# Performance work log

Hardware: AMD Instinct MI355X
Metric: run time of the kernel (lower is better)

Reference implementation:

```python
import jax, jax.numpy as jnp
import numpy as np

N = 50000          # nodes
E = 1_600_000      # edges (avg degree 32)
G = 512            # graphs in batch
IN_DIM = 128
HID = 64


def setup_inputs() -> dict:
    key = jax.random.key(0)
    ks = jax.random.split(key, 9)
    x = jax.random.normal(ks[0], (N, IN_DIM), dtype=jnp.float32)
    edge_index = jax.random.randint(ks[1], (2, E), 0, N, dtype=jnp.int64)
    edge_attr = jax.random.uniform(ks[2], (E,), dtype=jnp.float32)
    batch = jnp.sort(jax.random.randint(ks[3], (N,), 0, G, dtype=jnp.int64))
    W1 = jax.random.normal(ks[4], (IN_DIM, HID), dtype=jnp.float32) / np.sqrt(IN_DIM)
    b1 = jnp.zeros((HID,), dtype=jnp.float32)
    W2 = jax.random.normal(ks[5], (HID, HID), dtype=jnp.float32) / np.sqrt(HID)
    b2 = jnp.zeros((HID,), dtype=jnp.float32)
    Wlin = jax.random.normal(ks[6], (HID, 1), dtype=jnp.float32) / np.sqrt(HID)
    blin = jnp.zeros((1,), dtype=jnp.float32)
    return {"x": x, "edge_index": edge_index, "edge_attr": edge_attr,
            "batch": batch, "W1": W1, "b1": b1, "W2": W2, "b2": b2,
            "Wlin": Wlin, "blin": blin}


def reference(x, edge_index, edge_attr, batch, W1, b1, W2, b2, Wlin, blin):
    n = x.shape[0]
    src, dst = edge_index[0], edge_index[1]
    # GCNConv: add self-loops with weight 1, symmetric normalization
    loop = jnp.arange(n)
    src_f = jnp.concatenate([src, loop])
    dst_f = jnp.concatenate([dst, loop])
    w = jnp.concatenate([edge_attr, jnp.ones((n,), x.dtype)])
    deg = jax.ops.segment_sum(w, dst_f, num_segments=n)
    dis = jnp.where(deg > 0, jax.lax.rsqrt(jnp.maximum(deg, 1e-12)), 0.0)
    norm = dis[src_f] * w * dis[dst_f]  # [E+N]

    def conv(h, W, b):
        hw = h @ W                          # [N, HID]
        msg = norm[:, None] * hw[src_f]     # [E+N, HID]
        return jax.ops.segment_sum(msg, dst_f, num_segments=n) + b

    h = jax.nn.relu(conv(x, W1, b1))
    h = conv(h, W2, b2)
    # global_mean_pool over graph ids
    counts = jax.ops.segment_sum(jnp.ones((n,), h.dtype), batch, num_segments=G)
    pooled = jax.ops.segment_sum(h, batch, num_segments=G) / jnp.maximum(counts, 1.0)[:, None]
    return pooled @ Wlin + blin  # [G, 1]
```

## Files before the change

kernel.cpp:

```cpp
#include <hip/hip_runtime.h>

#define NN 50000
#define NE 1600000
#define NG 512
#define IN_DIM 128
#define HID 64

#define NB 128
#define NBK ((NN + NB - 1) / NB)
#define EBLK 250
#define EPB (NE / EBLK)
#define EPB4 (EPB / 4)

typedef unsigned short ushort_t;
typedef unsigned int uint_t;

static __device__ __forceinline__ ushort_t f2bf(float f) {
    uint_t u = __float_as_uint(f);
    u += 0x7FFFu + ((u >> 16) & 1u);
    return (ushort_t)(u >> 16);
}
static __device__ __forceinline__ float bflo(uint_t u) { return __uint_as_float(u << 16); }
static __device__ __forceinline__ float bfhi(uint_t u) { return __uint_as_float(u & 0xFFFF0000u); }

__global__ void cnt_kernel(const int* __restrict__ ei, int* __restrict__ pcnt) {
    __shared__ int h[NBK];
    for (int i = threadIdx.x; i < NBK; i += blockDim.x) h[i] = 0;
    __syncthreads();
    const int4* d4 = (const int4*)(ei + NE + blockIdx.x * EPB);
    for (int i = threadIdx.x; i < EPB4; i += blockDim.x) {
        int4 d = d4[i];
        atomicAdd(&h[d.x >> 7], 1);
        atomicAdd(&h[d.y >> 7], 1);
        atomicAdd(&h[d.z >> 7], 1);
        atomicAdd(&h[d.w >> 7], 1);
    }
    __syncthreads();
    for (int i = threadIdx.x; i < NBK; i += blockDim.x)
        pcnt[(size_t)i * EBLK + blockIdx.x] = h[i];
}

__global__ void bscan_kernel(int* __restrict__ pcnt, int* __restrict__ tot) {
    __shared__ int s[256];
    int k = blockIdx.x, t = threadIdx.x;
    int v = (t < EBLK) ? pcnt[(size_t)k * EBLK + t] : 0;
    s[t] = v;
    __syncthreads();
    for (int off = 1; off < 256; off <<= 1) {
        int add = (t >= off) ? s[t - off] : 0;
        __syncthreads();
        s[t] += add;
        __syncthreads();
    }
    if (t < EBLK) pcnt[(size_t)k * EBLK + t] = s[t] - v;
    if (t == 255) tot[k] = s[255];
}

__global__ void tscan_kernel(const int* __restrict__ tot, int* __restrict__ bbase) {
    __shared__ int s[512];
    int t = threadIdx.x;
    int v = (t < NBK) ? tot[t] : 0;
    s[t] = v;
    __syncthreads();
    for (int off = 1; off < 512; off <<= 1) {
        int add = (t >= off) ? s[t - off] : 0;
        __syncthreads();
        s[t] += add;
        __syncthreads();
    }
    if (t < NBK) bbase[t] = s[t] - v;
    if (t == NBK - 1) bbase[NBK] = s[t];
}

__global__ void scatter_kernel(const int* __restrict__ ei, const float* __restrict__ ea,
                               const int* __restrict__ pcnt, const int* __restrict__ bbase,
                               int2* __restrict__ recs) {
    __shared__ int curs[NBK];
    int b = blockIdx.x;
    for (int i = threadIdx.x; i < NBK; i += blockDim.x)
        curs[i] = bbase[i] + pcnt[(size_t)i * EBLK + b];
    __syncthreads();
    int base = b * EPB;
    const int4*   s4 = (const int4*)(ei + base);
    const int4*   d4 = (const int4*)(ei + NE + base);
    const float4* e4 = (const float4*)(ea + base);
    for (int i = threadIdx.x; i < EPB4; i += blockDim.x) {
        int4 ss = s4[i];
        int4 dd = d4[i];
        float4 ee = e4[i];
        int pos, k;
        k = dd.x >> 7; pos = atomicAdd(&curs[k], 1);
        recs[pos] = make_int2(((dd.x & 127) << 17) | ss.x, __float_as_int(ee.x));
        k = dd.y >> 7; pos = atomicAdd(&curs[k], 1);
        recs[pos] = make_int2(((dd.y & 127) << 17) | ss.y, __float_as_int(ee.y));
        k = dd.z >> 7; pos = atomicAdd(&curs[k], 1);
        recs[pos] = make_int2(((dd.z & 127) << 17) | ss.z, __float_as_int(ee.z));
        k = dd.w >> 7; pos = atomicAdd(&curs[k], 1);
        recs[pos] = make_int2(((dd.w & 127) << 17) | ss.w, __float_as_int(ee.w));
    }
}

__global__ void binfo2_kernel(const int2* __restrict__ recs, const int* __restrict__ bbase,
                              int* __restrict__ indeg, float* __restrict__ dis,
                              int* __restrict__ offs, int2* __restrict__ csr) {
    __shared__ float deg[NB];
    __shared__ int cnt[NB];
    __shared__ int sc[NB];
    __shared__ int curs[NB];
    __shared__ float wdst[NB];
    int k = blockIdx.x;
    int lo = k * NB;
    int nLoc = min(NB, NN - lo);
    int tid = threadIdx.x;
    for (int i = tid; i < nLoc; i += blockDim.x) { deg[i] = 0.f; cnt[i] = 0; }
    __syncthreads();
    int start = bbase[k], end = bbase[k + 1];
    for (int e = start + tid; e < end; e += blockDim.x) {
        int2 r = recs[e];
        int dl = r.x >> 17;
        atomicAdd(&deg[dl], __int_as_float(r.y));
        atomicAdd(&cnt[dl], 1);
    }
    __syncthreads();
    for (int i = tid; i < nLoc; i += blockDim.x) {
        float d = rsqrtf(deg[i] + 1.0f);
        wdst[i] = d;
        dis[lo + i] = d;
        indeg[lo + i] = cnt[i];
    }
    if (tid < NB) sc[tid] = (tid < nLoc) ? cnt[tid] : 0;
    __syncthreads();
    for (int off = 1; off < NB; off <<= 1) {
        int add = (tid < NB && tid >= off) ? sc[tid - off] : 0;
        __syncthreads();
        if (tid < NB) sc[tid] += add;
        __syncthreads();
    }
    if (tid < nLoc) {
        int ex = start + sc[tid] - cnt[tid];
        offs[lo + tid] = ex;
        curs[tid] = ex;
    }
    __syncthreads();
    for (int e = start + tid; e < end; e += blockDim.x) {
        int2 r = recs[e];
        int src = r.x & 0x1FFFF;
        int dl = r.x >> 17;
        float pw = __int_as_float(r.y) * wdst[dl];
        int pos = atomicAdd(&curs[dl], 1);
        csr[pos] = make_int2(src, __float_as_int(pw));
    }
}

template <int K>
__global__ __launch_bounds__(256) void gemm_kernel(const float* __restrict__ X,
                                                   const float* __restrict__ W,
                                                   const float* __restrict__ dis,
                                                   ushort_t* __restrict__ Yb) {
    __shared__ float w_lds[K * HID];
    __shared__ float x_lds[K][65];
    int tid = threadIdx.x;
    int rowbase = blockIdx.x * 64;
    for (int i = tid; i < K * HID; i += 256) w_lds[i] = W[i];
    for (int i = tid; i < 16 * K; i += 256) {
        int row = i / (K / 4);
        int k4 = i % (K / 4);
        int r = rowbase + row;
        float4 v = (r < NN) ? ((const float4*)(X + (size_t)r * K))[k4]
                            : make_float4(0.f, 0.f, 0.f, 0.f);
        x_lds[k4 * 4 + 0][row] = v.x;
        x_lds[k4 * 4 + 1][row] = v.y;
        x_lds[k4 * 4 + 2][row] = v.z;
        x_lds[k4 * 4 + 3][row] = v.w;
    }
    __syncthreads();
    int c0 = (tid & 15) * 4;
    int r0 = (tid >> 4) * 4;
    float acc[4][4] = {};
#pragma unroll 4
    for (int k = 0; k < K; ++k) {
        float x0 = x_lds[k][r0 + 0];
        float x1 = x_lds[k][r0 + 1];
        float x2 = x_lds[k][r0 + 2];
        float x3 = x_lds[k][r0 + 3];
        float4 wv = *(const float4*)&w_lds[k * HID + c0];
        acc[0][0] += x0 * wv.x; acc[0][1] += x0 * wv.y; acc[0][2] += x0 * wv.z; acc[0][3] += x0 * wv.w;
        acc[1][0] += x1 * wv.x; acc[1][1] += x1 * wv.y; acc[1][2] += x1 * wv.z; acc[1][3] += x1 * wv.w;
        acc[2][0] += x2 * wv.x; acc[2][1] += x2 * wv.y; acc[2][2] += x2 * wv.z; acc[2][3] += x2 * wv.w;
        acc[3][0] += x3 * wv.x; acc[3][1] += x3 * wv.y; acc[3][2] += x3 * wv.z; acc[3][3] += x3 * wv.w;
    }
#pragma unroll
    for (int i = 0; i < 4; ++i) {
        int r = rowbase + r0 + i;
        if (r < NN) {
            float dr = dis[r];
            ushort4 o;
            o.x = f2bf(dr * acc[i][0]); o.y = f2bf(dr * acc[i][1]);
            o.z = f2bf(dr * acc[i][2]); o.w = f2bf(dr * acc[i][3]);
            *(ushort4*)&Yb[(size_t)r * HID + c0] = o;
        }
    }
}

__global__ void gather1_kernel(const int2* __restrict__ csr,
                               const int* __restrict__ offs,
                               const int* __restrict__ indeg,
                               const float* __restrict__ dis,
                               const ushort_t* __restrict__ A1,
                               const float* __restrict__ b1,
                               float* __restrict__ OUT) {
    int node = blockIdx.x * 4 + (threadIdx.x >> 6);
    int lane = threadIdx.x & 63;
    if (node >= NN) return;
    int o  = lane >> 3;
    int cl = lane & 7;
    int start = offs[node];
    int n = indeg[node];
    float a0 = 0.f, a1 = 0.f, a2 = 0.f, a3 = 0.f;
    float a4 = 0.f, a5 = 0.f, a6 = 0.f, a7 = 0.f;
    for (int c = 0; c < n; c += 64) {
        int idx = c + lane;
        int2 rec = (idx < n) ? csr[start + idx] : make_int2(0, 0);
        int tmax = min(n - c, 64);
#pragma unroll 2
        for (int t = 0; t * 8 < tmax; ++t) {
            int sl = t * 8 + o;
            int key = __shfl(rec.x, sl, 64);
            float w = __int_as_float(__shfl(rec.y, sl, 64));
            uint4 v = *(const uint4*)(A1 + ((size_t)key << 6) + (cl << 3));
            a0 += w * bflo(v.x); a1 += w * bfhi(v.x);
            a2 += w * bflo(v.y); a3 += w * bfhi(v.y);
            a4 += w * bflo(v.z); a5 += w * bfhi(v.z);
            a6 += w * bflo(v.w); a7 += w * bfhi(v.w);
        }
    }
    a0 += __shfl_xor(a0, 8, 64); a0 += __shfl_xor(a0, 16, 64); a0 += __shfl_xor(a0, 32, 64);
    a1 += __shfl_xor(a1, 8, 64); a1 += __shfl_xor(a1, 16, 64); a1 += __shfl_xor(a1, 32, 64);
    a2 += __shfl_xor(a2, 8, 64); a2 += __shfl_xor(a2, 16, 64); a2 += __shfl_xor(a2, 32, 64);
    a3 += __shfl_xor(a3, 8, 64); a3 += __shfl_xor(a3, 16, 64); a3 += __shfl_xor(a3, 32, 64);
    a4 += __shfl_xor(a4, 8, 64); a4 += __shfl_xor(a4, 16, 64); a4 += __shfl_xor(a4, 32, 64);
    a5 += __shfl_xor(a5, 8, 64); a5 += __shfl_xor(a5, 16, 64); a5 += __shfl_xor(a5, 32, 64);
    a6 += __shfl_xor(a6, 8, 64); a6 += __shfl_xor(a6, 16, 64); a6 += __shfl_xor(a6, 32, 64);
    a7 += __shfl_xor(a7, 8, 64); a7 += __shfl_xor(a7, 16, 64); a7 += __shfl_xor(a7, 32, 64);
    if (o == 0) {
        float d = dis[node];
        uint4 sv = *(const uint4*)(A1 + ((size_t)node << 6) + (cl << 3));
        const float4* bv = (const float4*)(b1 + (cl << 3));
        float4 bA = bv[0], bB = bv[1];
        float o0 = fmaxf(a0 + d * bflo(sv.x) + bA.x, 0.f);
        float o1 = fmaxf(a1 + d * bfhi(sv.x) + bA.y, 0.f);
        float o2 = fmaxf(a2 + d * bflo(sv.y) + bA.z, 0.f);
        float o3 = fmaxf(a3 + d * bfhi(sv.y) + bA.w, 0.f);
        float o4 = fmaxf(a4 + d * bflo(sv.z) + bB.x, 0.f);
        float o5 = fmaxf(a5 + d * bfhi(sv.z) + bB.y, 0.f);
        float o6 = fmaxf(a6 + d * bflo(sv.w) + bB.z, 0.f);
        float o7 = fmaxf(a7 + d * bfhi(sv.w) + bB.w, 0.f);
        float* op = &OUT[((size_t)node << 6) + (cl << 3)];
        *(float4*)op       = make_float4(o0, o1, o2, o3);
        *(float4*)(op + 4) = make_float4(o4, o5, o6, o7);
    }
}

__global__ void gather2_kernel(const int2* __restrict__ csr,
                               const int* __restrict__ offs,
                               const int* __restrict__ indeg,
                               const float* __restrict__ dis,
                               const ushort_t* __restrict__ A2,
                               const float* __restrict__ b2,
                               const float* __restrict__ Wlin,
                               float* __restrict__ nodeval) {
    int node = blockIdx.x * 4 + (threadIdx.x >> 6);
    int lane = threadIdx.x & 63;
    if (node >= NN) return;
    int o  = lane >> 3;
    int cl = lane & 7;
    int start = offs[node];
    int n = indeg[node];
    float a0 = 0.f, a1 = 0.f, a2 = 0.f, a3 = 0.f;
    float a4 = 0.f, a5 = 0.f, a6 = 0.f, a7 = 0.f;
    for (int c = 0; c < n; c += 64) {
        int idx = c + lane;
        int2 rec = (idx < n) ? csr[start + idx] : make_int2(0, 0);
        int tmax = min(n - c, 64);
#pragma unroll 2
        for (int t = 0; t * 8 < tmax; ++t) {
            int sl = t * 8 + o;
            int key = __shfl(rec.x, sl, 64);
            float w = __int_as_float(__shfl(rec.y, sl, 64));
            uint4 v = *(const uint4*)(A2 + ((size_t)key << 6) + (cl << 3));
            a0 += w * bflo(v.x); a1 += w * bfhi(v.x);
            a2 += w * bflo(v.y); a3 += w * bfhi(v.y);
            a4 += w * bflo(v.z); a5 += w * bfhi(v.z);
            a6 += w * bflo(v.w); a7 += w * bfhi(v.w);
        }
    }
    a0 += __shfl_xor(a0, 8, 64); a0 += __shfl_xor(a0, 16, 64); a0 += __shfl_xor(a0, 32, 64);
    a1 += __shfl_xor(a1, 8, 64); a1 += __shfl_xor(a1, 16, 64); a1 += __shfl_xor(a1, 32, 64);
    a2 += __shfl_xor(a2, 8, 64); a2 += __shfl_xor(a2, 16, 64); a2 += __shfl_xor(a2, 32, 64);
    a3 += __shfl_xor(a3, 8, 64); a3 += __shfl_xor(a3, 16, 64); a3 += __shfl_xor(a3, 32, 64);
    a4 += __shfl_xor(a4, 8, 64); a4 += __shfl_xor(a4, 16, 64); a4 += __shfl_xor(a4, 32, 64);
    a5 += __shfl_xor(a5, 8, 64); a5 += __shfl_xor(a5, 16, 64); a5 += __shfl_xor(a5, 32, 64);
    a6 += __shfl_xor(a6, 8, 64); a6 += __shfl_xor(a6, 16, 64); a6 += __shfl_xor(a6, 32, 64);
    a7 += __shfl_xor(a7, 8, 64); a7 += __shfl_xor(a7, 16, 64); a7 += __shfl_xor(a7, 32, 64);
    float d = dis[node];
    uint4 sv = *(const uint4*)(A2 + ((size_t)node << 6) + (cl << 3));
    const float4* bv = (const float4*)(b2 + (cl << 3));
    float4 bA = bv[0], bB = bv[1];
    const float4* wv = (const float4*)(Wlin + (cl << 3));
    float4 wA = wv[0], wB = wv[1];
    float dot = (a0 + d * bflo(sv.x) + bA.x) * wA.x
              + (a1 + d * bfhi(sv.x) + bA.y) * wA.y
              + (a2 + d * bflo(sv.y) + bA.z) * wA.z
              + (a3 + d * bfhi(sv.y) + bA.w) * wA.w
              + (a4 + d * bflo(sv.z) + bB.x) * wB.x
              + (a5 + d * bfhi(sv.z) + bB.y) * wB.y
              + (a6 + d * bflo(sv.w) + bB.z) * wB.z
              + (a7 + d * bfhi(sv.w) + bB.w) * wB.w;
    dot += __shfl_xor(dot, 1, 64);
    dot += __shfl_xor(dot, 2, 64);
    dot += __shfl_xor(dot, 4, 64);
    if (lane == 0) nodeval[node] = dot;
}

__global__ void pool_final_kernel(const float* __restrict__ nodeval,
                                  const int* __restrict__ batch,
                                  const float* __restrict__ blin,
                                  float* __restrict__ out) {
    __shared__ int bnd[2];
    __shared__ float red[4];
    int g = blockIdx.x;
    if (threadIdx.x < 2) {
        int target = g + threadIdx.x;
        int lo = 0, hi = NN;
        while (lo < hi) {
            int mid = (lo + hi) >> 1;
            if (batch[mid] < target) lo = mid + 1; else hi = mid;
        }
        bnd[threadIdx.x] = lo;
    }
    __syncthreads();
    int s = bnd[0], e = bnd[1];
    float a = 0.f;
    for (int i = s + threadIdx.x; i < e; i += 256) a += nodeval[i];
    for (int off = 32; off > 0; off >>= 1) a += __shfl_down(a, off, 64);
    int lane = threadIdx.x & 63;
    int wv = threadIdx.x >> 6;
    if (lane == 0) red[wv] = a;
    __syncthreads();
    if (threadIdx.x == 0) {
        float t = red[0] + red[1] + red[2] + red[3];
        out[g] = t / fmaxf((float)(e - s), 1.0f) + blin[0];
    }
}

extern "C" void kernel_launch(void* const* d_in, const int* in_sizes, int n_in,
                              void* d_out, int out_size, void* d_ws, size_t ws_size,
                              hipStream_t stream) {
    const float* x     = (const float*)d_in[0];
    const int*   ei    = (const int*)d_in[1];
    const float* ea    = (const float*)d_in[2];
    const int*   batch = (const int*)d_in[3];
    const float* W1    = (const float*)d_in[4];
    const float* b1    = (const float*)d_in[5];
    const float* W2    = (const float*)d_in[6];
    const float* b2    = (const float*)d_in[7];
    const float* Wlin  = (const float*)d_in[8];
    const float* blin  = (const float*)d_in[9];
    float*       out   = (float*)d_out;

    char* ws = (char*)d_ws;
    auto alloc = [&](size_t bytes) {
        void* p = (void*)ws;
        ws += (bytes + 255) / 256 * 256;
        return p;
    };
    float*    dis     = (float*)alloc((size_t)NN * 4);
    int*      indeg   = (int*)alloc((size_t)NN * 4);
    int*      offs    = (int*)alloc((size_t)NN * 4);
    int*      pcnt    = (int*)alloc((size_t)NBK * EBLK * 4);
    int*      tot     = (int*)alloc((size_t)NBK * 4);
    int*      bbase   = (int*)alloc((size_t)(NBK + 1) * 4);
    int2*     recs    = (int2*)alloc((size_t)NE * 8);
    int2*     csr     = (int2*)alloc((size_t)NE * 8);
    float*    B       = (float*)alloc((size_t)NN * HID * 4);
    float*    nodeval = (float*)alloc((size_t)NN * 4);
    ushort_t* A1      = (ushort_t*)recs;
    ushort_t* A2      = (ushort_t*)recs + (size_t)NN * HID;

    cnt_kernel<<<EBLK, 256, 0, stream>>>(ei, pcnt);
    bscan_kernel<<<NBK, 256, 0, stream>>>(pcnt, tot);
    tscan_kernel<<<1, 512, 0, stream>>>(tot, bbase);
    scatter_kernel<<<EBLK, 256, 0, stream>>>(ei, ea, pcnt, bbase, recs);
    binfo2_kernel<<<NBK, 256, 0, stream>>>(recs, bbase, indeg, dis, offs, csr);

    gemm_kernel<IN_DIM><<<(NN + 63) / 64, 256, 0, stream>>>(x, W1, dis, A1);
    gather1_kernel<<<(NN + 3) / 4, 256, 0, stream>>>(csr, offs, indeg, dis, A1, b1, B);

    gemm_kernel<HID><<<(NN + 63) / 64, 256, 0, stream>>>(B, W2, dis, A2);
    gather2_kernel<<<(NN + 3) / 4, 256, 0, stream>>>(csr, offs, indeg, dis, A2, b2,
                                                     Wlin, nodeval);

    pool_final_kernel<<<NG, 256, 0, stream>>>(nodeval, batch, blin, out);
}
```

Baseline: 153.7 us.

## Stage CSR bucket in LDS, store hidden layer as bf16, drop indeg array

The CSR build now scatters each 128-node bucket into shared memory and then writes it out to global memory coalesced, instead of doing random global stores. It falls back to the old path when a bucket holds more than 6144 edges. The layer-1 output is stored as bf16 rather than fp32, and a new GEMM kernel reads that bf16 input, halving that intermediate's traffic. The indeg array is replaced by an N+1 offsets array. The bf16 hidden layer adds rounding error, and the 48KB LDS stage may reduce occupancy of the binfo kernel.

```diff
diff --git a/kernel.cpp b/kernel.cpp
--- a/kernel.cpp
+++ b/kernel.cpp
@@ -11,6 +11,7 @@
 #define EBLK 250
 #define EPB (NE / EBLK)
 #define EPB4 (EPB / 4)
+#define BCAP 6144
 
 typedef unsigned short ushort_t;
 typedef unsigned int uint_t;
@@ -101,32 +102,33 @@
 }
 
 __global__ void binfo2_kernel(const int2* __restrict__ recs, const int* __restrict__ bbase,
-                              int* __restrict__ indeg, float* __restrict__ dis,
-                              int* __restrict__ offs, int2* __restrict__ csr) {
+                              float* __restrict__ dis, int* __restrict__ offs,
+                              int2* __restrict__ csr) {
     __shared__ float deg[NB];
     __shared__ int cnt[NB];
     __shared__ int sc[NB];
     __shared__ int curs[NB];
     __shared__ float wdst[NB];
+    __shared__ int2 stage[BCAP];
     int k = blockIdx.x;
     int lo = k * NB;
     int nLoc = min(NB, NN - lo);
     int tid = threadIdx.x;
-    for (int i = tid; i < nLoc; i += blockDim.x) { deg[i] = 0.f; cnt[i] = 0; }
+    for (int i = tid; i < nLoc; i += 256) { deg[i] = 0.f; cnt[i] = 0; }
     __syncthreads();
     int start = bbase[k], end = bbase[k + 1];
-    for (int e = start + tid; e < end; e += blockDim.x) {
-        int2 r = recs[e];
+    int m = end - start;
+    for (int e = tid; e < m; e += 256) {
+        int2 r = recs[start + e];
         int dl = r.x >> 17;
         atomicAdd(&deg[dl], __int_as_float(r.y));
         atomicAdd(&cnt[dl], 1);
     }
     __syncthreads();
-    for (int i = tid; i < nLoc; i += blockDim.x) {
+    for (int i = tid; i < nLoc; i += 256) {
         float d = rsqrtf(deg[i] + 1.0f);
         wdst[i] = d;
         dis[lo + i] = d;
-        indeg[lo + i] = cnt[i];
     }
     if (tid < NB) sc[tid] = (tid < nLoc) ? cnt[tid] : 0;
     __syncthreads();
@@ -137,18 +139,33 @@
         __syncthreads();
     }
     if (tid < nLoc) {
-        int ex = start + sc[tid] - cnt[tid];
-        offs[lo + tid] = ex;
-        curs[tid] = ex;
-    }
-    __syncthreads();
-    for (int e = start + tid; e < end; e += blockDim.x) {
-        int2 r = recs[e];
-        int src = r.x & 0x1FFFF;
-        int dl = r.x >> 17;
-        float pw = __int_as_float(r.y) * wdst[dl];
-        int pos = atomicAdd(&curs[dl], 1);
-        csr[pos] = make_int2(src, __float_as_int(pw));
+        int exRel = sc[tid] - cnt[tid];
+        offs[lo + tid] = start + exRel;
+        curs[tid] = exRel;
+    }
+    if (k == NBK - 1 && tid == 0) offs[NN] = end;
+    __syncthreads();
+    if (m <= BCAP) {
+        for (int e = tid; e < m; e += 256) {
+            int2 r = recs[start + e];
+            int src = r.x & 0x1FFFF;
+            int dl = r.x >> 17;
+            float pw = __int_as_float(r.y) * wdst[dl];
+            int pos = atomicAdd(&curs[dl], 1);
+            stage[pos] = make_int2(src, __float_as_int(pw));
+        }
+        __syncthreads();
+        for (int e = tid; e < m; e += 256)
+            csr[start + e] = stage[e];
+    } else {
+        for (int e = tid; e < m; e += 256) {
+            int2 r = recs[start + e];
+            int src = r.x & 0x1FFFF;
+            int dl = r.x >> 17;
+            float pw = __int_as_float(r.y) * wdst[dl];
+            int pos = atomicAdd(&curs[dl], 1);
+            csr[start + pos] = make_int2(src, __float_as_int(pw));
+        }
     }
 }
 
@@ -202,20 +219,69 @@
     }
 }
 
+__global__ __launch_bounds__(256) void gemm2b_kernel(const ushort_t* __restrict__ Xb,
+                                                     const float* __restrict__ W,
+                                                     const float* __restrict__ dis,
+                                                     ushort_t* __restrict__ Yb) {
+    __shared__ float w_lds[HID * HID];
+    __shared__ float x_lds[HID][65];
+    int tid = threadIdx.x;
+    int rowbase = blockIdx.x * 64;
+    for (int i = tid; i < HID * HID; i += 256) w_lds[i] = W[i];
+    for (int i = tid; i < 512; i += 256) {
+        int row = i >> 3;
+        int g = i & 7;
+        int r = rowbase + row;
+        uint4 v = make_uint4(0u, 0u, 0u, 0u);
+        if (r < NN) v = ((const uint4*)(Xb + ((size_t)r << 6)))[g];
+        int k0 = g * 8;
+        x_lds[k0 + 0][row] = bflo(v.x); x_lds[k0 + 1][row] = bfhi(v.x);
+        x_lds[k0 + 2][row] = bflo(v.y); x_lds[k0 + 3][row] = bfhi(v.y);
+        x_lds[k0 + 4][row] = bflo(v.z); x_lds[k0 + 5][row] = bfhi(v.z);
+        x_lds[k0 + 6][row] = bflo(v.w); x_lds[k0 + 7][row] = bfhi(v.w);
+    }
+    __syncthreads();
+    int c0 = (tid & 15) * 4;
+    int r0 = (tid >> 4) * 4;
+    float acc[4][4] = {};
+#pragma unroll 4
+    for (int k = 0; k < HID; ++k) {
+        float x0 = x_lds[k][r0 + 0];
+        float x1 = x_lds[k][r0 + 1];
+        float x2 = x_lds[k][r0 + 2];
+        float x3 = x_lds[k][r0 + 3];
+        float4 wv = *(const float4*)&w_lds[k * HID + c0];
+        acc[0][0] += x0 * wv.x; acc[0][1] += x0 * wv.y; acc[0][2] += x0 * wv.z; acc[0][3] += x0 * wv.w;
+        acc[1][0] += x1 * wv.x; acc[1][1] += x1 * wv.y; acc[1][2] += x1 * wv.z; acc[1][3] += x1 * wv.w;
+        acc[2][0] += x2 * wv.x; acc[2][1] += x2 * wv.y; acc[2][2] += x2 * wv.z; acc[2][3] += x2 * wv.w;
+        acc[3][0] += x3 * wv.x; acc[3][1] += x3 * wv.y; acc[3][2] += x3 * wv.z; acc[3][3] += x3 * wv.w;
+    }
+#pragma unroll
+    for (int i = 0; i < 4; ++i) {
+        int r = rowbase + r0 + i;
+        if (r < NN) {
+            float dr = dis[r];
+            ushort4 o;
+            o.x = f2bf(dr * acc[i][0]); o.y = f2bf(dr * acc[i][1]);
+            o.z = f2bf(dr * acc[i][2]); o.w = f2bf(dr * acc[i][3]);
+            *(ushort4*)&Yb[(size_t)r * HID + c0] = o;
+        }
+    }
+}
+
 __global__ void gather1_kernel(const int2* __restrict__ csr,
                                const int* __restrict__ offs,
-                               const int* __restrict__ indeg,
                                const float* __restrict__ dis,
                                const ushort_t* __restrict__ A1,
                                const float* __restrict__ b1,
-                               float* __restrict__ OUT) {
+                               ushort_t* __restrict__ H1b) {
     int node = blockIdx.x * 4 + (threadIdx.x >> 6);
     int lane = threadIdx.x & 63;
     if (node >= NN) return;
     int o  = lane >> 3;
     int cl = lane & 7;
     int start = offs[node];
-    int n = indeg[node];
+    int n = offs[node + 1] - start;
     float a0 = 0.f, a1 = 0.f, a2 = 0.f, a3 = 0.f;
     float a4 = 0.f, a5 = 0.f, a6 = 0.f, a7 = 0.f;
     for (int c = 0; c < n; c += 64) {
@@ -255,15 +321,17 @@
         float o5 = fmaxf(a5 + d * bfhi(sv.z) + bB.y, 0.f);
         float o6 = fmaxf(a6 + d * bflo(sv.w) + bB.z, 0.f);
         float o7 = fmaxf(a7 + d * bfhi(sv.w) + bB.w, 0.f);
-        float* op = &OUT[((size_t)node << 6) + (cl << 3)];
-        *(float4*)op       = make_float4(o0, o1, o2, o3);
-        *(float4*)(op + 4) = make_float4(o4, o5, o6, o7);
+        uint4 ov;
+        ov.x = (uint_t)f2bf(o0) | ((uint_t)f2bf(o1) << 16);
+        ov.y = (uint_t)f2bf(o2) | ((uint_t)f2bf(o3) << 16);
+        ov.z = (uint_t)f2bf(o4) | ((uint_t)f2bf(o5) << 16);
+        ov.w = (uint_t)f2bf(o6) | ((uint_t)f2bf(o7) << 16);
+        *(uint4*)(H1b + ((size_t)node << 6) + (cl << 3)) = ov;
     }
 }
 
 __global__ void gather2_kernel(const int2* __restrict__ csr,
                                const int* __restrict__ offs,
-                               const int* __restrict__ indeg,
                                const float* __restrict__ dis,
                                const ushort_t* __restrict__ A2,
                                const float* __restrict__ b2,
@@ -275,7 +343,7 @@
     int o  = lane >> 3;
     int cl = lane & 7;
     int start = offs[node];
-    int n = indeg[node];
+    int n = offs[node + 1] - start;
     float a0 = 0.f, a1 = 0.f, a2 = 0.f, a3 = 0.f;
     float a4 = 0.f, a5 = 0.f, a6 = 0.f, a7 = 0.f;
     for (int c = 0; c < n; c += 64) {
@@ -375,14 +443,13 @@
         return p;
     };
     float*    dis     = (float*)alloc((size_t)NN * 4);
-    int*      indeg   = (int*)alloc((size_t)NN * 4);
-    int*      offs    = (int*)alloc((size_t)NN * 4);
+    int*      offs    = (int*)alloc((size_t)(NN + 1) * 4);
     int*      pcnt    = (int*)alloc((size_t)NBK * EBLK * 4);
     int*      tot     = (int*)alloc((size_t)NBK * 4);
     int*      bbase   = (int*)alloc((size_t)(NBK + 1) * 4);
     int2*     recs    = (int2*)alloc((size_t)NE * 8);
     int2*     csr     = (int2*)alloc((size_t)NE * 8);
-    float*    B       = (float*)alloc((size_t)NN * HID * 4);
+    ushort_t* H1b     = (ushort_t*)alloc((size_t)NN * HID * 2);
     float*    nodeval = (float*)alloc((size_t)NN * 4);
     ushort_t* A1      = (ushort_t*)recs;
     ushort_t* A2      = (ushort_t*)recs + (size_t)NN * HID;
@@ -391,13 +458,13 @@
     bscan_kernel<<<NBK, 256, 0, stream>>>(pcnt, tot);
     tscan_kernel<<<1, 512, 0, stream>>>(tot, bbase);
     scatter_kernel<<<EBLK, 256, 0, stream>>>(ei, ea, pcnt, bbase, recs);
-    binfo2_kernel<<<NBK, 256, 0, stream>>>(recs, bbase, indeg, dis, offs, csr);
+    binfo2_kernel<<<NBK, 256, 0, stream>>>(recs, bbase, dis, offs, csr);
 
     gemm_kernel<IN_DIM><<<(NN + 63) / 64, 256, 0, stream>>>(x, W1, dis, A1);
-    gather1_kernel<<<(NN + 3) / 4, 256, 0, stream>>>(csr, offs, indeg, dis, A1, b1, B);
-
-    gemm_kernel<HID><<<(NN + 63) / 64, 256, 0, stream>>>(B, W2, dis, A2);
-    gather2_kernel<<<(NN + 3) / 4, 256, 0, stream>>>(csr, offs, indeg, dis, A2, b2,
+    gather1_kernel<<<(NN + 3) / 4, 256, 0, stream>>>(csr, offs, dis, A1, b1, H1b);
+
+    gemm2b_kernel<<<(NN + 63) / 64, 256, 0, stream>>>(H1b, W2, dis, A2);
+    gather2_kernel<<<(NN + 3) / 4, 256, 0, stream>>>(csr, offs, dis, A2, b2,
                                                      Wlin, nodeval);
 
     pool_final_kernel<<<NG, 256, 0, stream>>>(nodeval, batch, blin, out);
```

Result: faster. 148.6 us, median of 2 (-3.3%).
